# Optimization experiments

Hardware: AMD Instinct MI355X
Metric: run time of the kernel (lower is better)

The kernel has to match this reference:

```python
import jax, jax.numpy as jnp
import numpy as np
from jax import lax

BASE = 10000.0

def _rope(x):
    # x: (b, h, w, c). Faithful to torch RoPE: angles depend only on one spatial
    # axis (h,k_max) and broadcast against the *w* axis of x (valid since h==w).
    b, h, w, c = x.shape
    k_max = c // 2
    theta = 1.0 / (BASE ** (jnp.arange(k_max, dtype=x.dtype) / k_max))  # (k_max,)
    angles = jnp.arange(h, dtype=x.dtype)[:, None] * theta              # (h, k_max)
    cos = jnp.cos(angles)[None, None]  # (1,1,h,k_max) -> broadcasts over w axis
    sin = jnp.sin(angles)[None, None]
    xr = x.reshape(b, h, w, k_max, 2)
    re, im = xr[..., 0], xr[..., 1]
    out = jnp.stack([re * cos - im * sin, re * sin + im * cos], axis=-1)
    return out.reshape(b, h, w, c)


def setup_inputs() -> dict:
    key = jax.random.key(0)
    k1, k2, k3 = jax.random.split(key, 3)
    B, C, H, W = 8, 128, 160, 160
    x = jax.random.normal(k1, (B, C, H, W), dtype=jnp.float32)
    qk_w = jax.random.normal(k2, (2 * C, C), dtype=jnp.float32) * 0.02
    qk_b = jnp.zeros((2 * C,), dtype=jnp.float32)
    lepe_w = jax.random.normal(k3, (C, 1, 3, 3), dtype=jnp.float32) * 0.1
    lepe_b = jnp.zeros((C,), dtype=jnp.float32)
    return {"x": x, "qk_w": qk_w, "qk_b": qk_b,
            "lepe_w": lepe_w, "lepe_b": lepe_b, "num_heads": 8}


def reference(x, qk_w, qk_b, lepe_w, lepe_b, num_heads):
    b, c, H, W = x.shape
    n = H * W
    hd = c // num_heads
    # raw row-major reshape (B,C,H,W) -> (B,N,C), matching torch .reshape
    xf = x.reshape(b, n, c)
    qk = (xf @ qk_w.T + qk_b).reshape(b, n, 2, c)
    q = jax.nn.elu(qk[:, :, 0]) + 1.0
    k = jax.nn.elu(qk[:, :, 1]) + 1.0
    v = xf
    q_rope = _rope(q.reshape(b, H, W, c)).reshape(b, n, num_heads, hd).transpose(0, 2, 1, 3)
    k_rope = _rope(k.reshape(b, H, W, c)).reshape(b, n, num_heads, hd).transpose(0, 2, 1, 3)
    qh = q.reshape(b, n, num_heads, hd).transpose(0, 2, 1, 3)  # (b,h,n,d)
    kh = k.reshape(b, n, num_heads, hd).transpose(0, 2, 1, 3)
    vh = v.reshape(b, n, num_heads, hd).transpose(0, 2, 1, 3)
    z = 1.0 / (jnp.einsum('bhnd,bhd->bhn', qh, kh.mean(axis=2)) + 1e-6)  # (b,h,n)
    scale = float(n) ** -0.5
    kv = jnp.einsum('bhnd,bhne->bhde', k_rope * scale, vh * scale)  # (b,h,d,d)
    out = jnp.einsum('bhnd,bhde->bhne', q_rope, kv) * z[..., None]  # (b,h,n,d)
    out = out.transpose(0, 2, 1, 3).reshape(b, n, c)
    # LePE: depthwise 3x3 conv on v laid out as image
    vimg = vh.transpose(0, 2, 1, 3).reshape(b, H, W, c).transpose(0, 3, 1, 2)  # (b,c,H,W)
    lepe = lax.conv_general_dilated(vimg, lepe_w, (1, 1), 'SAME',
                                    feature_group_count=c)
    lepe = lepe + lepe_b[None, :, None, None]
    out = out + lepe.transpose(0, 2, 3, 1).reshape(b, n, c)
    return out.transpose(0, 2, 1).reshape(b, c, H, W)
```

## Files before the change

### kernel.cpp

```cpp
#include <hip/hip_runtime.h>
#include <cstdint>
#include <cstddef>

#define NB 8
#define NC 128
#define NHH 160
#define NWW 160
#define NNN (NHH*NWW)
#define TILE_R 64
#define TPB (NNN/TILE_R)
#define NSLOTS 32
#define LN_B 0.14391156511f

typedef __attribute__((ext_vector_type(8))) short short8v;
typedef __attribute__((ext_vector_type(4))) short short4v;
typedef __attribute__((ext_vector_type(4))) float f32x4;
union B64x2 { short8v v8; short4v v4[2]; ushort u[8]; uint w[4]; };

__device__ __forceinline__ float elup1(float y){ return y>0.f? y+1.f : __expf(y); }
__device__ __forceinline__ ushort f2bf(float f){ uint x=__float_as_uint(f); x+=0x7fffu+((x>>16)&1u); return (ushort)(x>>16); }
__device__ __forceinline__ uint cvtpk(float lo, float hi){
  uint r;
  asm("v_cvt_pk_bf16_f32 %0, %1, %2" : "=v"(r) : "v"(lo), "v"(hi));
  return r;
}
__device__ __forceinline__ float frcp(float x){
  float r;
  asm("v_rcp_f32 %0, %1" : "=v"(r) : "v"(x));
  return r;
}
__device__ __forceinline__ float bfhi(uint u){ return __uint_as_float(u & 0xffff0000u); }
__device__ __forceinline__ float bflo(uint u){ return __uint_as_float(u << 16); }
__device__ __forceinline__ int divH(int i){ return ((i >> 5) * 6554) >> 15; }
__device__ __forceinline__ int iclamp(int v, int lo, int hi){ return v<lo?lo:(v>hi?hi:v); }

__global__ __launch_bounds__(256) void kprep(
    const float* __restrict__ qk_w, ushort* __restrict__ wbf,
    float2* __restrict__ rtab, float* __restrict__ zreg)
{
  const int id = blockIdx.x*256 + threadIdx.x;
  if (id < 2*NC*NC) wbf[id] = f2bf(qk_w[id]);
  if (id < NWW*64) {
    const int ww = id >> 6, f = id & 63;
    const float th = __expf(-LN_B * (float)f);
    float s, c; __sincosf((float)ww * th, &s, &c);
    rtab[id] = make_float2(c, s);
  }
  #pragma unroll
  for (int j = 0; j < 17; ++j)
    zreg[id + j*32768] = 0.f;
}

__global__ __launch_bounds__(256, 4) void k1_proj(
    const float* __restrict__ x, const ushort* __restrict__ wbf,
    const float* __restrict__ qk_b, const float2* __restrict__ rtab,
    ushort* __restrict__ qu, float* __restrict__ kv_part,
    float* __restrict__ ksum_part)
{
  __shared__ __align__(16) ushort xbf[64][136];
  __shared__ __align__(16) ushort wch[64][136];
  __shared__ float ksum_lds[NC];
  ushort* xtp = &wch[0][0];
  ushort* krt = &wch[0][0] + 4352;

  const int blk  = ((blockIdx.x & 7) * (NB*TPB/8)) + (blockIdx.x >> 3);
  const int b    = blk / TPB;
  const int tile = blk - b * TPB;
  const int i0   = tile * TILE_R;
  const int tid  = threadIdx.x;
  const int lane = tid & 63;
  const int wv   = tid >> 6;
  const int lg   = lane >> 4;
  const int ll   = lane & 15;
  const float* xb = x + (size_t)b*NNN*NC + (size_t)i0*NC;

  {
    const float4* src = (const float4*)xb;
    for (int f = tid; f < TILE_R*NC/4; f += 256) {
      float4 v = src[f];
      uint w0 = cvtpk(v.x, v.y), w1 = cvtpk(v.z, v.w);
      *(uint2*)&xbf[f >> 5][(f & 31) << 2] = make_uint2(w0, w1);
    }
  }
  if (tid < NC) ksum_lds[tid] = 0.f;

  f32x4 kvacc[2];
  kvacc[0] = (f32x4){0.f,0.f,0.f,0.f};
  kvacc[1] = (f32x4){0.f,0.f,0.f,0.f};
  const int row0 = (wv<<4) + (lg<<2);

  int wfr4[4];
  #pragma unroll
  for (int r = 0; r < 4; ++r) {
    const int i = i0 + row0 + r;
    wfr4[r] = i - divH(i)*NWW;
  }

  for (int chunk = 0; chunk < 4; ++chunk) {
    if (chunk) __syncthreads();
    {
      const uint4* wsrc = (const uint4*)(wbf + (size_t)(chunk*64)*NC);
      for (int f = tid; f < 1024; f += 256)
        *(uint4*)&wch[f >> 4][(f & 15) << 3] = wsrc[f];
    }
    __syncthreads();

    f32x4 acc[4];
    acc[0]=acc[1]=acc[2]=acc[3]=(f32x4){0.f,0.f,0.f,0.f};
    #pragma unroll
    for (int ks = 0; ks < 4; ++ks) {
      short8v a = *(const short8v*)&xbf[(wv<<4) + ll][(ks<<5) + (lg<<3)];
      #pragma unroll
      for (int nt = 0; nt < 4; ++nt) {
        short8v bb = *(const short8v*)&wch[(nt<<4) + ll][(ks<<5) + (lg<<3)];
        acc[nt] = __builtin_amdgcn_mfma_f32_16x16x32_bf16(a, bb, acc[nt], 0, 0, 0);
      }
    }

    if (chunk < 2) {
      ushort* qb = qu + ((size_t)b*NNN + (size_t)i0)*NC;
      #pragma unroll
      for (int nt = 0; nt < 4; ++nt) {
        const int cg = (chunk<<6) + (nt<<4) + ll;
        const float bias = qk_b[cg];
        #pragma unroll
        for (int r = 0; r < 4; ++r)
          qb[(size_t)(row0 + r)*NC + cg] = f2bf(elup1(acc[nt][r] + bias));
      }
    } else {
      uint rbw[4][2];
      #pragma unroll
      for (int nt = 0; nt < 4; ++nt) {
        const int kc = ((chunk-2)<<6) + (nt<<4) + ll;
        const float bias = qk_b[NC + kc];
        float kk[4]; float ss = 0.f;
        #pragma unroll
        for (int r = 0; r < 4; ++r) { kk[r] = elup1(acc[nt][r] + bias); ss += kk[r]; }
        atomicAdd(&ksum_lds[kc], ss);
        ushort rb[4];
        #pragma unroll
        for (int r = 0; r < 4; ++r) {
          float p = __shfl_xor(kk[r], 1);
          float2 cs = rtab[wfr4[r]*64 + (kc >> 1)];
          float kr = (kc & 1) ? (p*cs.y + kk[r]*cs.x) : (kk[r]*cs.x - p*cs.y);
          rb[r] = f2bf(kr);
        }
        rbw[nt][0] = (uint)rb[0] | ((uint)rb[1] << 16);
        rbw[nt][1] = (uint)rb[2] | ((uint)rb[3] << 16);
      }
      __syncthreads();

      #pragma unroll
      for (int nt = 0; nt < 4; ++nt) {
        const int kcl = (nt<<4) + ll;
        *(uint*)&krt[kcl*68 + row0]     = rbw[nt][0];
        *(uint*)&krt[kcl*68 + row0 + 2] = rbw[nt][1];
      }
      #pragma unroll
      for (int t = 0; t < 2; ++t) {
        const int task = tid + (t << 8);
        const int c = task & 63, rg = task >> 6;
        ushort tmp[8];
        #pragma unroll
        for (int k2 = 0; k2 < 8; ++k2) tmp[k2] = xbf[(rg<<3)+k2][((chunk-2)<<6)+c];
        *(ushort4*)&xtp[c*68 + (rg<<3)]     = make_ushort4(tmp[0],tmp[1],tmp[2],tmp[3]);
        *(ushort4*)&xtp[c*68 + (rg<<3) + 4] = make_ushort4(tmp[4],tmp[5],tmp[6],tmp[7]);
      }
      __syncthreads();

      const int e2 = chunk - 2;
      #pragma unroll
      for (int ks = 0; ks < 2; ++ks) {
        const int rb2 = (ks<<5) + (lg<<3);
        B64x2 ua, ub;
        ua.v4[0] = *(const short4v*)&krt[((wv<<4) + ll)*68 + rb2];
        ua.v4[1] = *(const short4v*)&krt[((wv<<4) + ll)*68 + rb2 + 4];
        ub.v4[0] = *(const short4v*)&xtp[((wv<<4) + ll)*68 + rb2];
        ub.v4[1] = *(const short4v*)&xtp[((wv<<4) + ll)*68 + rb2 + 4];
        kvacc[e2] = __builtin_amdgcn_mfma_f32_16x16x32_bf16(ua.v8, ub.v8, kvacc[e2], 0, 0, 0);
      }
    }
  }

  const int slot = blk & (NSLOTS-1);
  {
    float* kvp = kv_part + ((size_t)b*NSLOTS + slot) * 2048;
    #pragma unroll
    for (int e2 = 0; e2 < 2; ++e2) {
      const int h = (e2<<2) + wv;
      #pragma unroll
      for (int r = 0; r < 4; ++r) {
        const int d = (lg<<2) + r;
        atomicAdd(&kvp[(h<<8) + (d<<4) + ll], kvacc[e2][r]);
      }
    }
  }
  __syncthreads();
  if (tid < NC) atomicAdd(&ksum_part[((size_t)b*NSLOTS + slot)*NC + tid], ksum_lds[tid]);
}

__global__ __launch_bounds__(256) void k_reduce(
    const float* __restrict__ kv_part, const float* __restrict__ ksum_part,
    float* __restrict__ kvf, float* __restrict__ kmean)
{
  const int gtid = blockIdx.x * 256 + threadIdx.x;
  const int b = gtid >> 11;
  const int cidx = gtid & 2047;
  float s = 0.f;
  for (int sl = 0; sl < NSLOTS; ++sl)
    s += kv_part[((size_t)b*NSLOTS + sl)*2048 + cidx];
  kvf[(size_t)b*2048 + cidx] = s * (1.f/25600.f);
  if (cidx < NC) {
    float t = 0.f;
    for (int sl = 0; sl < NSLOTS; ++sl)
      t += ksum_part[((size_t)b*NSLOTS + sl)*NC + cidx];
    kmean[(size_t)b*NC + cidx] = t * (1.f/25600.f);
  }
}

__global__ __launch_bounds__(256, 2) void k2_out(
    const float* __restrict__ x, const ushort* __restrict__ qu,
    const float* __restrict__ kvf, const float* __restrict__ kmean,
    const float* __restrict__ lepe_w, const float* __restrict__ lepe_b,
    const float2* __restrict__ rtab, float* __restrict__ outp)
{
  __shared__ __align__(16) ushort qu_s[64*136];

  const int blk  = ((blockIdx.x & 7) * (NB*TPB/8)) + (blockIdx.x >> 3);
  const int b    = blk / TPB;
  const int tile = blk - b * TPB;
  const int i0   = tile * TILE_R;
  const int tid  = threadIdx.x;
  const int lane = tid & 63;
  const int wv   = tid >> 6;
  const int lg   = lane >> 4;
  const int ll   = lane & 15;
  const float* xb = x + (size_t)b*NNN*NC;

  {
    const uint4* qsrc = (const uint4*)(qu + ((size_t)b*NNN + (size_t)i0)*NC);
    #pragma unroll
    for (int t = 0; t < 4; ++t) {
      const int f = tid + (t << 8);
      uint4 v = qsrc[f];
      const int row = f >> 4, c8 = f & 15;
      *(uint4*)&qu_s[row*136 + ((c8 ^ (row & 7)) << 3)] = v;
    }
  }
  __syncthreads();

  const bool interior = (i0 >= 192) && (i0 <= NNN - 225);

  int wfa[4];
  #pragma unroll
  for (int mt = 0; mt < 4; ++mt) {
    const int i = i0 + (mt<<4) + ll;
    wfa[mt] = i - divH(i)*NWW;
  }

  #pragma unroll
  for (int hs = 0; hs < 2; ++hs) {
    const int h  = wv + (hs<<2);
    const int ch = (h<<4) + ll;
    B64x2 kb, kz;
    kb.v8 = (short8v){0,0,0,0,0,0,0,0};
    kz.v8 = (short8v){0,0,0,0,0,0,0,0};
    if (lg < 2) {
      const float* kvp = kvf + (size_t)b*2048 + (h<<8) + ll;
      #pragma unroll
      for (int j2 = 0; j2 < 4; ++j2) {
        float f0 = kvp[(((lg<<3) + 2*j2    ) << 4)];
        float f1 = kvp[(((lg<<3) + 2*j2 + 1) << 4)];
        kb.w[j2] = cvtpk(f0, f1);
      }
      const float* kmp = kmean + (size_t)b*NC + (h<<4) + (lg<<3);
      #pragma unroll
      for (int j2 = 0; j2 < 4; ++j2)
        kz.w[j2] = cvtpk(kmp[2*j2], kmp[2*j2+1]);
    }
    f32x4 pacc[4], zacc[4];
    #pragma unroll
    for (int mt = 0; mt < 4; ++mt) {
      short8v a  = (short8v){0,0,0,0,0,0,0,0};
      short8v au = (short8v){0,0,0,0,0,0,0,0};
      if (lg < 2) {
        const int row = (mt<<4) + ll;
        const int off = row*136 + ((((h<<1) + lg) ^ (row & 7)) << 3);
        B64x2 uq;
        uq.v8 = *(const short8v*)&qu_s[off];
        au = uq.v8;
        const float2* tp = rtab + wfa[mt]*64 + (h<<3) + (lg<<2);
        B64x2 ra;
        #pragma unroll
        for (int j = 0; j < 4; ++j) {
          float2 cs = tp[j];
          float e = bflo(uq.w[j]), o = bfhi(uq.w[j]);
          ra.w[j] = cvtpk(e*cs.x - o*cs.y, e*cs.y + o*cs.x);
        }
        a = ra.v8;
      }
      pacc[mt] = __builtin_amdgcn_mfma_f32_16x16x32_bf16(
          a,  kb.v8, (f32x4){0.f,0.f,0.f,0.f}, 0, 0, 0);
      zacc[mt] = __builtin_amdgcn_mfma_f32_16x16x32_bf16(
          au, kz.v8, (f32x4){0.f,0.f,0.f,0.f}, 0, 0, 0);
    }
    float wl[9];
    #pragma unroll
    for (int t = 0; t < 9; ++t) wl[t] = lepe_w[ch*9 + t];
    const float lb = lepe_b[ch];
    const float* xc = xb + ch;

    if (interior) {
      #pragma unroll
      for (int mt = 0; mt < 4; ++mt) {
        const int lrow = (mt<<4) + (lg<<2);
        const int ib   = i0 + lrow;
        const float* pu = xc + (size_t)(ib-161)*NC;
        const float* pm = xc + (size_t)(ib-1  )*NC;
        const float* pd = xc + (size_t)(ib+159)*NC;
        float mu[6], mm[6], md[6];
        #pragma unroll
        for (int j = 0; j < 6; ++j) {
          mu[j] = pu[j*NC]; mm[j] = pm[j*NC]; md[j] = pd[j*NC];
        }
        int ww = ib - divH(ib)*NWW;
        float4 ov;
        #pragma unroll
        for (int r = 0; r < 4; ++r) {
          const float zz = frcp(zacc[mt][r] + 1e-6f);
          const float fx0 = ww > 0   ? 1.f : 0.f;
          const float fx2 = ww < 159 ? 1.f : 0.f;
          float lp = lb;
          lp += fx0*(wl[0]*mu[r] + wl[3]*mm[r] + wl[6]*md[r]);
          lp +=     (wl[1]*mu[r+1] + wl[4]*mm[r+1] + wl[7]*md[r+1]);
          lp += fx2*(wl[2]*mu[r+2] + wl[5]*mm[r+2] + wl[8]*md[r+2]);
          (&ov.x)[r] = pacc[mt][r]*zz + lp;
          ww = (ww == NWW-1) ? 0 : ww + 1;
        }
        *(float4*)(outp + ((size_t)b*NC + ch)*NNN + ib) = ov;
      }
    } else {
      #pragma unroll
      for (int mt = 0; mt < 4; ++mt) {
        const int lrow = (mt<<4) + (lg<<2);
        const int ib   = i0 + lrow;
        float mu[6], mm[6], md[6];
        #pragma unroll
        for (int j = 0; j < 6; ++j) {
          const int im = ib - 1 + j;
          mu[j] = xc[(size_t)(iclamp(im-160, 0, NNN-1)) * NC];
          mm[j] = xc[(size_t)(iclamp(im,     0, NNN-1)) * NC];
          md[j] = xc[(size_t)(iclamp(im+160, 0, NNN-1)) * NC];
        }
        int hh = divH(ib);
        int ww = ib - hh*NWW;
        float4 ov;
        #pragma unroll
        for (int r = 0; r < 4; ++r) {
          const float zz = frcp(zacc[mt][r] + 1e-6f);
          const float fy0 = hh > 0   ? 1.f : 0.f;
          const float fy2 = hh < 159 ? 1.f : 0.f;
          const float fx0 = ww > 0   ? 1.f : 0.f;
          const float fx2 = ww < 159 ? 1.f : 0.f;
          float lp = lb;
          lp += fy0*(fx0*wl[0]*mu[r] + wl[1]*mu[r+1] + fx2*wl[2]*mu[r+2]);
          lp +=     (fx0*wl[3]*mm[r] + wl[4]*mm[r+1] + fx2*wl[5]*mm[r+2]);
          lp += fy2*(fx0*wl[6]*md[r] + wl[7]*md[r+1] + fx2*wl[8]*md[r+2]);
          (&ov.x)[r] = pacc[mt][r]*zz + lp;
          const int cy = (ww == NWW-1) ? 1 : 0;
          hh += cy;
          ww = cy ? 0 : ww + 1;
        }
        *(float4*)(outp + ((size_t)b*NC + ch)*NNN + ib) = ov;
      }
    }
  }
}

extern "C" void kernel_launch(void* const* d_in, const int* in_sizes, int n_in,
                              void* d_out, int out_size, void* d_ws, size_t ws_size,
                              hipStream_t stream) {
  const float* x      = (const float*)d_in[0];
  const float* qk_w   = (const float*)d_in[1];
  const float* qk_b   = (const float*)d_in[2];
  const float* lepe_w = (const float*)d_in[3];
  const float* lepe_b = (const float*)d_in[4];
  float* outp = (float*)d_out;

  float* kv_part   = (float*)d_ws;
  float* ksum_part = kv_part + (size_t)NB*NSLOTS*2048;
  float* kvf       = ksum_part + (size_t)NB*NSLOTS*NC;
  float* kmean     = kvf + (size_t)NB*2048;
  float2* rtab     = (float2*)(kmean + (size_t)NB*NC);
  ushort* wbf      = (ushort*)(rtab + (size_t)NWW*64);
  ushort* qubuf    = wbf + (size_t)2*NC*NC;

  hipLaunchKernelGGL(kprep, dim3(128), dim3(256), 0, stream,
                     qk_w, wbf, rtab, kv_part);
  hipLaunchKernelGGL(k1_proj, dim3(NB*TPB), dim3(256), 0, stream,
                     x, wbf, qk_b, rtab, qubuf, kv_part, ksum_part);
  hipLaunchKernelGGL(k_reduce, dim3(64), dim3(256), 0, stream,
                     kv_part, ksum_part, kvf, kmean);
  hipLaunchKernelGGL(k2_out, dim3(NB*TPB), dim3(256), 0, stream,
                     x, qubuf, kvf, kmean, lepe_w, lepe_b, rtab, outp);
}
```

Before: 157.4 us.

## Swizzle k1_proj LDS tiles and reduce k column sums via shuffles

```diff
diff --git a/kernel.cpp b/kernel.cpp
--- a/kernel.cpp
+++ b/kernel.cpp
@@ -33,6 +33,8 @@
 __device__ __forceinline__ float bflo(uint u){ return __uint_as_float(u << 16); }
 __device__ __forceinline__ int divH(int i){ return ((i >> 5) * 6554) >> 15; }
 __device__ __forceinline__ int iclamp(int v, int lo, int hi){ return v<lo?lo:(v>hi?hi:v); }
+__device__ __forceinline__ int sw16(int row, int cb){ return (row<<7) + ((cb ^ (row & 7)) << 3); }
+__device__ __forceinline__ int sw8 (int row, int cb){ return (row<<6) + ((cb ^ (row & 7)) << 2); }
 
 __global__ __launch_bounds__(256) void kprep(
     const float* __restrict__ qk_w, ushort* __restrict__ wbf,
@@ -57,11 +59,10 @@
     ushort* __restrict__ qu, float* __restrict__ kv_part,
     float* __restrict__ ksum_part)
 {
-  __shared__ __align__(16) ushort xbf[64][136];
-  __shared__ __align__(16) ushort wch[64][136];
-  __shared__ float ksum_lds[NC];
-  ushort* xtp = &wch[0][0];
-  ushort* krt = &wch[0][0] + 4352;
+  __shared__ __align__(16) ushort xbf[64*128];
+  __shared__ __align__(16) ushort wch[64*128];
+  ushort* xtp = wch;
+  ushort* krt = wch + 4096;
 
   const int blk  = ((blockIdx.x & 7) * (NB*TPB/8)) + (blockIdx.x >> 3);
   const int b    = blk / TPB;
@@ -72,6 +73,7 @@
   const int wv   = tid >> 6;
   const int lg   = lane >> 4;
   const int ll   = lane & 15;
+  const int slot = blk & (NSLOTS-1);
   const float* xb = x + (size_t)b*NNN*NC + (size_t)i0*NC;
 
   {
@@ -79,14 +81,17 @@
     for (int f = tid; f < TILE_R*NC/4; f += 256) {
       float4 v = src[f];
       uint w0 = cvtpk(v.x, v.y), w1 = cvtpk(v.z, v.w);
-      *(uint2*)&xbf[f >> 5][(f & 31) << 2] = make_uint2(w0, w1);
-    }
-  }
-  if (tid < NC) ksum_lds[tid] = 0.f;
+      const int row = f >> 5, q = f & 31;
+      *(uint2*)&xbf[sw16(row, q >> 1) + ((q & 1) << 2)] = make_uint2(w0, w1);
+    }
+  }
 
   f32x4 kvacc[2];
   kvacc[0] = (f32x4){0.f,0.f,0.f,0.f};
   kvacc[1] = (f32x4){0.f,0.f,0.f,0.f};
+  float ssv[8];
+  #pragma unroll
+  for (int t = 0; t < 8; ++t) ssv[t] = 0.f;
   const int row0 = (wv<<4) + (lg<<2);
 
   int wfr4[4];
@@ -101,7 +106,7 @@
     {
       const uint4* wsrc = (const uint4*)(wbf + (size_t)(chunk*64)*NC);
       for (int f = tid; f < 1024; f += 256)
-        *(uint4*)&wch[f >> 4][(f & 15) << 3] = wsrc[f];
+        *(uint4*)&wch[sw16(f >> 4, f & 15)] = wsrc[f];
     }
     __syncthreads();
 
@@ -109,10 +114,10 @@
     acc[0]=acc[1]=acc[2]=acc[3]=(f32x4){0.f,0.f,0.f,0.f};
     #pragma unroll
     for (int ks = 0; ks < 4; ++ks) {
-      short8v a = *(const short8v*)&xbf[(wv<<4) + ll][(ks<<5) + (lg<<3)];
+      short8v a = *(const short8v*)&xbf[sw16((wv<<4) + ll, (ks<<2) + lg)];
       #pragma unroll
       for (int nt = 0; nt < 4; ++nt) {
-        short8v bb = *(const short8v*)&wch[(nt<<4) + ll][(ks<<5) + (lg<<3)];
+        short8v bb = *(const short8v*)&wch[sw16((nt<<4) + ll, (ks<<2) + lg)];
         acc[nt] = __builtin_amdgcn_mfma_f32_16x16x32_bf16(a, bb, acc[nt], 0, 0, 0);
       }
     }
@@ -136,7 +141,7 @@
         float kk[4]; float ss = 0.f;
         #pragma unroll
         for (int r = 0; r < 4; ++r) { kk[r] = elup1(acc[nt][r] + bias); ss += kk[r]; }
-        atomicAdd(&ksum_lds[kc], ss);
+        ssv[((chunk-2)<<2) + nt] = ss;
         ushort rb[4];
         #pragma unroll
         for (int r = 0; r < 4; ++r) {
@@ -153,36 +158,38 @@
       #pragma unroll
       for (int nt = 0; nt < 4; ++nt) {
         const int kcl = (nt<<4) + ll;
-        *(uint*)&krt[kcl*68 + row0]     = rbw[nt][0];
-        *(uint*)&krt[kcl*68 + row0 + 2] = rbw[nt][1];
+        const int base = sw8(kcl, row0 >> 2);
+        *(uint*)&krt[base]     = rbw[nt][0];
+        *(uint*)&krt[base + 2] = rbw[nt][1];
       }
       #pragma unroll
       for (int t = 0; t < 2; ++t) {
         const int task = tid + (t << 8);
         const int c = task & 63, rg = task >> 6;
+        const int col = ((chunk-2)<<6) + c;
         ushort tmp[8];
         #pragma unroll
-        for (int k2 = 0; k2 < 8; ++k2) tmp[k2] = xbf[(rg<<3)+k2][((chunk-2)<<6)+c];
-        *(ushort4*)&xtp[c*68 + (rg<<3)]     = make_ushort4(tmp[0],tmp[1],tmp[2],tmp[3]);
-        *(ushort4*)&xtp[c*68 + (rg<<3) + 4] = make_ushort4(tmp[4],tmp[5],tmp[6],tmp[7]);
+        for (int k2 = 0; k2 < 8; ++k2)
+          tmp[k2] = xbf[sw16((rg<<3) + k2, col >> 3) + (col & 7)];
+        *(ushort4*)&xtp[sw8(c, (rg<<1)    )] = make_ushort4(tmp[0],tmp[1],tmp[2],tmp[3]);
+        *(ushort4*)&xtp[sw8(c, (rg<<1) + 1)] = make_ushort4(tmp[4],tmp[5],tmp[6],tmp[7]);
       }
       __syncthreads();
 
       const int e2 = chunk - 2;
       #pragma unroll
       for (int ks = 0; ks < 2; ++ks) {
-        const int rb2 = (ks<<5) + (lg<<3);
+        const int cb = (ks<<3) + (lg<<1);
         B64x2 ua, ub;
-        ua.v4[0] = *(const short4v*)&krt[((wv<<4) + ll)*68 + rb2];
-        ua.v4[1] = *(const short4v*)&krt[((wv<<4) + ll)*68 + rb2 + 4];
-        ub.v4[0] = *(const short4v*)&xtp[((wv<<4) + ll)*68 + rb2];
-        ub.v4[1] = *(const short4v*)&xtp[((wv<<4) + ll)*68 + rb2 + 4];
+        ua.v4[0] = *(const short4v*)&krt[sw8((wv<<4) + ll, cb    )];
+        ua.v4[1] = *(const short4v*)&krt[sw8((wv<<4) + ll, cb + 1)];
+        ub.v4[0] = *(const short4v*)&xtp[sw8((wv<<4) + ll, cb    )];
+        ub.v4[1] = *(const short4v*)&xtp[sw8((wv<<4) + ll, cb + 1)];
         kvacc[e2] = __builtin_amdgcn_mfma_f32_16x16x32_bf16(ua.v8, ub.v8, kvacc[e2], 0, 0, 0);
       }
     }
   }
 
-  const int slot = blk & (NSLOTS-1);
   {
     float* kvp = kv_part + ((size_t)b*NSLOTS + slot) * 2048;
     #pragma unroll
@@ -195,8 +202,17 @@
       }
     }
   }
-  __syncthreads();
-  if (tid < NC) atomicAdd(&ksum_part[((size_t)b*NSLOTS + slot)*NC + tid], ksum_lds[tid]);
+  {
+    float* kbase = ksum_part + ((size_t)b*NSLOTS + slot)*NC;
+    #pragma unroll
+    for (int t = 0; t < 8; ++t) {
+      float s = ssv[t];
+      s += __shfl_xor(s, 16);
+      s += __shfl_xor(s, 32);
+      if (lg == 0)
+        atomicAdd(&kbase[((t>>2)<<6) + ((t&3)<<4) + ll], s);
+    }
+  }
 }
 
 __global__ __launch_bounds__(256) void k_reduce(
```

After: 159.0 us. About the same (+1.0%).
